# Kernel optimization log

Measured on AMD Instinct MI355X. Metric: run time of the kernel, lower is better.

The kernel has to match this reference:

```python
import jax, jax.numpy as jnp
import numpy as np

N = 50000      # nodes
K = 17         # regular degree (edges per node, pre-sorted by row)
D_IN = 128
D_OUT = 64
E = N * K


def setup_inputs() -> dict:
    key = jax.random.key(0)
    k1, k2, k3, k4, k5 = jax.random.split(key, 5)
    x = jax.random.normal(k1, (N, D_IN), dtype=jnp.float32)
    # edges sorted by row (required by dimmedian_idx); regular degree K
    row = jnp.repeat(jnp.arange(N, dtype=jnp.int32), K)
    col = jax.random.randint(k2, (E,), 0, N, dtype=jnp.int32)
    edge_index = jnp.stack([row, col], axis=0)
    edge_weight = jax.random.uniform(k3, (E,), dtype=jnp.float32)
    # glorot-style linear weight, zero-init-like small bias
    weight = jax.random.normal(k4, (D_IN, D_OUT), dtype=jnp.float32) * np.float32(1.0 / np.sqrt(D_IN))
    bias = jax.random.normal(k5, (D_OUT,), dtype=jnp.float32) * np.float32(0.01)
    return {"x": x, "edge_index": edge_index, "edge_weight": edge_weight,
            "weight": weight, "bias": bias}


def _weighted_dim_median(xp, col, w):
    """Per-node, per-dimension weighted median over neighbors (dimmedian_idx + gather).
    xp: [N, D] projected features; col: [E] neighbor ids; w: [E] edge weights.
    Exploits the regular degree K: edges for node i occupy rows i*K:(i+1)*K.
    """
    D = xp.shape[1]
    vals = xp[col].reshape(N, K, D)            # neighbor features per node
    wN = jnp.broadcast_to(w.reshape(N, K)[:, :, None], (N, K, D))
    order = jnp.argsort(vals, axis=1)          # sort neighbors per dim by value
    sorted_vals = jnp.take_along_axis(vals, order, axis=1)
    sorted_w = jnp.take_along_axis(wN, order, axis=1)
    cum = jnp.cumsum(sorted_w, axis=1)
    total = cum[:, -1:, :]
    # first sorted position where cumulative weight reaches half the total
    med_pos = jnp.argmax(cum >= 0.5 * total, axis=1)      # [N, D]
    med = jnp.take_along_axis(sorted_vals, med_pos[:, None, :], axis=1)[:, 0, :]
    return med


def reference(x, edge_index, edge_weight, weight, bias):
    xp = x @ weight                            # lin projection (no bias)
    row, col = edge_index[0], edge_index[1]
    med = _weighted_dim_median(xp, col, edge_weight)      # soft_median_reduce
    # row normalization: scatter_add of edge weights per destination row
    row_sum = jax.ops.segment_sum(edge_weight, row, num_segments=N)
    return row_sum[:, None] * med + bias
```

## Files before the change

### kernel.cpp

```cpp
#include <hip/hip_runtime.h>

#define N_NODES 50000
#define K_DEG   17
#define DIN     128
#define DOUT    64

struct CEPair { unsigned char a, b; };

constexpr int net_count(int n) {
  int t = 0; while ((1 << t) < n) ++t;
  int cnt = 0;
  for (int p = 1 << (t - 1); p > 0; p >>= 1) {
    int q = 1 << (t - 1), r = 0, d = p;
    for (;;) {
      for (int i = 0; i < n - d; ++i)
        if ((i & p) == r) ++cnt;
      if (q == p) break;
      d = q - p; q >>= 1; r = p;
    }
  }
  return cnt;
}

template <int NP>
struct NetArr { CEPair v[NP]; };

template <int NP>
constexpr NetArr<NP> net_pairs(int n) {
  NetArr<NP> out{};
  int t = 0; while ((1 << t) < n) ++t;
  int cnt = 0;
  for (int p = 1 << (t - 1); p > 0; p >>= 1) {
    int q = 1 << (t - 1), r = 0, d = p;
    for (;;) {
      for (int i = 0; i < n - d; ++i)
        if ((i & p) == r) {
          out.v[cnt].a = (unsigned char)i;
          out.v[cnt].b = (unsigned char)(i + d);
          ++cnt;
        }
      if (q == p) break;
      d = q - p; q >>= 1; r = p;
    }
  }
  return out;
}

constexpr int NP17 = net_count(K_DEG);

__global__ __launch_bounds__(256) void gemm_kernel(
    const float* __restrict__ x, const float* __restrict__ W,
    float* __restrict__ xp) {
  __shared__ float Wl[DIN * DOUT];
  {
    const float4* Wg4 = (const float4*)W;
    float4* Wl4 = (float4*)Wl;
    #pragma unroll
    for (int i = 0; i < (DIN * DOUT / 4) / 256; ++i)
      Wl4[threadIdx.x + i * 256] = Wg4[threadIdx.x + i * 256];
  }
  __syncthreads();

  const int t  = threadIdx.x;
  const int d0 = (t & 15) * 4;
  const int rg = t >> 4;
  const int r0 = blockIdx.x * 64 + rg * 4;

  float4 acc[4];
  #pragma unroll
  for (int rr = 0; rr < 4; ++rr) acc[rr] = make_float4(0.f, 0.f, 0.f, 0.f);

  int rbase[4];
  #pragma unroll
  for (int rr = 0; rr < 4; ++rr) {
    int r = r0 + rr;
    rbase[rr] = (r < N_NODES ? r : N_NODES - 1) * (DIN / 4);
  }

  const float4* x4 = (const float4*)x;
  for (int kc = 0; kc < DIN / 4; ++kc) {
    float4 xv[4];
    #pragma unroll
    for (int rr = 0; rr < 4; ++rr) xv[rr] = x4[rbase[rr] + kc];
    #pragma unroll
    for (int kk = 0; kk < 4; ++kk) {
      float4 wv = *(const float4*)&Wl[(kc * 4 + kk) * DOUT + d0];
      #pragma unroll
      for (int rr = 0; rr < 4; ++rr) {
        float xs = (kk == 0) ? xv[rr].x : (kk == 1) ? xv[rr].y
                 : (kk == 2) ? xv[rr].z : xv[rr].w;
        acc[rr].x += xs * wv.x;
        acc[rr].y += xs * wv.y;
        acc[rr].z += xs * wv.z;
        acc[rr].w += xs * wv.w;
      }
    }
  }
  #pragma unroll
  for (int rr = 0; rr < 4; ++rr) {
    int r = r0 + rr;
    if (r < N_NODES) *(float4*)&xp[r * DOUT + d0] = acc[rr];
  }
}

__global__ __launch_bounds__(256) void median_kernel(
    const float* __restrict__ xp, const int* __restrict__ col,
    const float* __restrict__ ew, const float* __restrict__ bias,
    float* __restrict__ out) {
  const int wave = threadIdx.x >> 6;
  const int lane = threadIdx.x & 63;
  const int node = blockIdx.x * 4 + wave;
  if (node >= N_NODES) return;

  const int*   cp = col + node * K_DEG;
  const float* wp = ew  + node * K_DEG;

  float v[K_DEG], w[K_DEG];
  #pragma unroll
  for (int j = 0; j < K_DEG; ++j) {
    int c = cp[j];
    v[j] = xp[c * DOUT + lane];
    w[j] = wp[j];
  }

  float rs = 0.f;
  #pragma unroll
  for (int j = 0; j < K_DEG; ++j) rs += w[j];

  constexpr NetArr<NP17> NET = net_pairs<NP17>(K_DEG);
  #pragma unroll
  for (int s = 0; s < NP17; ++s) {
    const int a = NET.v[s].a, b = NET.v[s].b;
    float va = v[a], vb = v[b];
    bool sw = vb < va;
    float wa = w[a], wb = w[b];
    v[a] = sw ? vb : va;  v[b] = sw ? va : vb;
    w[a] = sw ? wb : wa;  w[b] = sw ? wa : wb;
  }

  float tot = 0.f;
  #pragma unroll
  for (int j = 0; j < K_DEG; ++j) tot += w[j];
  const float half = 0.5f * tot;

  float cum = 0.f, med = 0.f;
  bool found = false;
  #pragma unroll
  for (int j = 0; j < K_DEG; ++j) {
    cum += w[j];
    bool ge  = (cum >= half);
    bool hit = ge && !found;
    med   = hit ? v[j] : med;
    found = found || ge;
  }

  out[node * DOUT + lane] = rs * med + bias[lane];
}

extern "C" void kernel_launch(void* const* d_in, const int* in_sizes, int n_in,
                              void* d_out, int out_size, void* d_ws, size_t ws_size,
                              hipStream_t stream) {
  const float* x    = (const float*)d_in[0];
  const int*   ei   = (const int*)d_in[1];
  const float* ew   = (const float*)d_in[2];
  const float* W    = (const float*)d_in[3];
  const float* bias = (const float*)d_in[4];
  float*       out  = (float*)d_out;
  float*       xp   = (float*)d_ws;
  const int*   colp = ei + (size_t)N_NODES * K_DEG;

  gemm_kernel<<<(N_NODES + 63) / 64, 256, 0, stream>>>(x, W, xp);
  median_kernel<<<(N_NODES + 3) / 4, 256, 0, stream>>>(xp, colp, ew, bias, out);
}
```

Before: 140.8 us.

## Use split-bf16 MFMA for projection GEMM and simplify median selection

Replaces the fp32 FMA projection GEMM with bf16 MFMA 16x16x32 instructions. Both x and W are split into high and low bf16 parts, and three MFMAs (hi*hi, hi*lo, lo*hi) approximate fp32 accuracy. W is stored transposed and padded in shared memory, and each wave computes a 16-row tile. The median scan is also rewritten as a prefix-sum array plus a reverse select chain, which removes the separate total sum and the found flag. The three-term split drops the lo*lo term, so a small precision risk remains, and median order ties could shift the selected element.

```diff
diff --git a/kernel.cpp b/kernel.cpp
--- a/kernel.cpp
+++ b/kernel.cpp
@@ -4,6 +4,10 @@
 #define K_DEG   17
 #define DIN     128
 #define DOUT    64
+#define KP      136
+
+typedef __attribute__((ext_vector_type(8))) short  short8;
+typedef __attribute__((ext_vector_type(4))) float  floatx4;
 
 struct CEPair { unsigned char a, b; };
 
@@ -22,8 +26,7 @@
   return cnt;
 }
 
-template <int NP>
-struct NetArr { CEPair v[NP]; };
+template <int NP> struct NetArr { CEPair v[NP]; };
 
 template <int NP>
 constexpr NetArr<NP> net_pairs(int n) {
@@ -48,58 +51,102 @@
 
 constexpr int NP17 = net_count(K_DEG);
 
+__device__ __forceinline__ unsigned int f2bf(float f) {
+  union { float f; unsigned int u; } c; c.f = f;
+  return (c.u + 0x7FFFu + ((c.u >> 16) & 1u)) >> 16;
+}
+__device__ __forceinline__ float bf2f(unsigned int b) {
+  union { float f; unsigned int u; } c; c.u = b << 16;
+  return c.f;
+}
+
 __global__ __launch_bounds__(256) void gemm_kernel(
     const float* __restrict__ x, const float* __restrict__ W,
     float* __restrict__ xp) {
-  __shared__ float Wl[DIN * DOUT];
+  __shared__ unsigned short Wht[DOUT * KP];
+  __shared__ unsigned short Wlt[DOUT * KP];
+
+  const int t = threadIdx.x;
+
   {
     const float4* Wg4 = (const float4*)W;
-    float4* Wl4 = (float4*)Wl;
-    #pragma unroll
-    for (int i = 0; i < (DIN * DOUT / 4) / 256; ++i)
-      Wl4[threadIdx.x + i * 256] = Wg4[threadIdx.x + i * 256];
+    #pragma unroll
+    for (int i = 0; i < 8; ++i) {
+      int fi  = t + i * 256;
+      int idx = fi * 4;
+      int k   = idx >> 6;
+      int n0  = idx & 63;
+      float4 wv = Wg4[fi];
+      float  f[4] = {wv.x, wv.y, wv.z, wv.w};
+      #pragma unroll
+      for (int e = 0; e < 4; ++e) {
+        unsigned int hb = f2bf(f[e]);
+        float        lo = f[e] - bf2f(hb);
+        unsigned int lb = f2bf(lo);
+        Wht[(n0 + e) * KP + k] = (unsigned short)hb;
+        Wlt[(n0 + e) * KP + k] = (unsigned short)lb;
+      }
+    }
   }
   __syncthreads();
 
-  const int t  = threadIdx.x;
-  const int d0 = (t & 15) * 4;
-  const int rg = t >> 4;
-  const int r0 = blockIdx.x * 64 + rg * 4;
-
-  float4 acc[4];
-  #pragma unroll
-  for (int rr = 0; rr < 4; ++rr) acc[rr] = make_float4(0.f, 0.f, 0.f, 0.f);
-
-  int rbase[4];
-  #pragma unroll
-  for (int rr = 0; rr < 4; ++rr) {
-    int r = r0 + rr;
-    rbase[rr] = (r < N_NODES ? r : N_NODES - 1) * (DIN / 4);
-  }
+  const int wid   = t >> 6;
+  const int lane  = t & 63;
+  const int gwave = blockIdx.x * 4 + wid;
+  if (gwave >= (N_NODES / 16)) return;
+
+  const int r0 = gwave * 16;
+  const int m  = lane & 15;
+  const int q  = lane >> 4;
 
   const float4* x4 = (const float4*)x;
-  for (int kc = 0; kc < DIN / 4; ++kc) {
-    float4 xv[4];
-    #pragma unroll
-    for (int rr = 0; rr < 4; ++rr) xv[rr] = x4[rbase[rr] + kc];
-    #pragma unroll
-    for (int kk = 0; kk < 4; ++kk) {
-      float4 wv = *(const float4*)&Wl[(kc * 4 + kk) * DOUT + d0];
-      #pragma unroll
-      for (int rr = 0; rr < 4; ++rr) {
-        float xs = (kk == 0) ? xv[rr].x : (kk == 1) ? xv[rr].y
-                 : (kk == 2) ? xv[rr].z : xv[rr].w;
-        acc[rr].x += xs * wv.x;
-        acc[rr].y += xs * wv.y;
-        acc[rr].z += xs * wv.z;
-        acc[rr].w += xs * wv.w;
-      }
-    }
-  }
-  #pragma unroll
-  for (int rr = 0; rr < 4; ++rr) {
-    int r = r0 + rr;
-    if (r < N_NODES) *(float4*)&xp[r * DOUT + d0] = acc[rr];
+  float4 xr[8];
+  #pragma unroll
+  for (int ks = 0; ks < 4; ++ks) {
+    int base = (r0 + m) * (DIN / 4) + ks * 8 + q * 2;
+    xr[ks * 2 + 0] = x4[base + 0];
+    xr[ks * 2 + 1] = x4[base + 1];
+  }
+
+  floatx4 acc[4];
+  #pragma unroll
+  for (int nt = 0; nt < 4; ++nt) acc[nt] = (floatx4){0.f, 0.f, 0.f, 0.f};
+
+  const int nb = lane & 15;
+
+  #pragma unroll
+  for (int ks = 0; ks < 4; ++ks) {
+    float f[8] = {xr[ks*2].x, xr[ks*2].y, xr[ks*2].z, xr[ks*2].w,
+                  xr[ks*2+1].x, xr[ks*2+1].y, xr[ks*2+1].z, xr[ks*2+1].w};
+    union { unsigned int i[4]; short8 s; } Ah, Al;
+    #pragma unroll
+    for (int r = 0; r < 4; ++r) {
+      unsigned int h0 = f2bf(f[2*r]),   h1 = f2bf(f[2*r+1]);
+      unsigned int l0 = f2bf(f[2*r]   - bf2f(h0));
+      unsigned int l1 = f2bf(f[2*r+1] - bf2f(h1));
+      Ah.i[r] = h0 | (h1 << 16);
+      Al.i[r] = l0 | (l1 << 16);
+    }
+    const int kk = ks * 32 + q * 8;
+    #pragma unroll
+    for (int nt = 0; nt < 4; ++nt) {
+      const int n = nt * 16 + nb;
+      short8 Bh = *(const short8*)&Wht[n * KP + kk];
+      short8 Bl = *(const short8*)&Wlt[n * KP + kk];
+      acc[nt] = __builtin_amdgcn_mfma_f32_16x16x32_bf16(Al.s, Bh, acc[nt], 0, 0, 0);
+      acc[nt] = __builtin_amdgcn_mfma_f32_16x16x32_bf16(Ah.s, Bl, acc[nt], 0, 0, 0);
+      acc[nt] = __builtin_amdgcn_mfma_f32_16x16x32_bf16(Ah.s, Bh, acc[nt], 0, 0, 0);
+    }
+  }
+
+  #pragma unroll
+  for (int nt = 0; nt < 4; ++nt) {
+    const int col = nt * 16 + nb;
+    #pragma unroll
+    for (int r = 0; r < 4; ++r) {
+      const int row = r0 + q * 4 + r;
+      xp[row * DOUT + col] = acc[nt][r];
+    }
   }
 }
 
@@ -138,21 +185,16 @@
     w[a] = sw ? wb : wa;  w[b] = sw ? wa : wb;
   }
 
-  float tot = 0.f;
-  #pragma unroll
-  for (int j = 0; j < K_DEG; ++j) tot += w[j];
-  const float half = 0.5f * tot;
-
-  float cum = 0.f, med = 0.f;
-  bool found = false;
-  #pragma unroll
-  for (int j = 0; j < K_DEG; ++j) {
-    cum += w[j];
-    bool ge  = (cum >= half);
-    bool hit = ge && !found;
-    med   = hit ? v[j] : med;
-    found = found || ge;
-  }
+  float c[K_DEG];
+  float run = 0.f;
+  #pragma unroll
+  for (int j = 0; j < K_DEG; ++j) { run += w[j]; c[j] = run; }
+  const float half = 0.5f * run;
+
+  float med = v[K_DEG - 1];
+  #pragma unroll
+  for (int j = K_DEG - 2; j >= 0; --j)
+    med = (c[j] >= half) ? v[j] : med;
 
   out[node * DOUT + lane] = rs * med + bias[lane];
 }
@@ -169,6 +211,7 @@
   float*       xp   = (float*)d_ws;
   const int*   colp = ei + (size_t)N_NODES * K_DEG;
 
-  gemm_kernel<<<(N_NODES + 63) / 64, 256, 0, stream>>>(x, W, xp);
+  const int nwaves = N_NODES / 16;
+  gemm_kernel<<<(nwaves + 3) / 4, 256, 0, stream>>>(x, W, xp);
   median_kernel<<<(N_NODES + 3) / 4, 256, 0, stream>>>(xp, colp, ew, bias, out);
 }
```

Result: faster. 131.3 us (-6.7%).
